# Optimization experiments

Measured on AMD Instinct MI355X. Metric: run time of the kernel, lower is better.

The kernel has to match this reference:

```python
import jax, jax.numpy as jnp
import numpy as np

D_MODEL = 1024
NUM_HEADS = 16
D_K = D_MODEL // NUM_HEADS
ROPE_THETA = 10000.0


def setup_inputs() -> dict:
    key = jax.random.key(0)
    kx, kq, kk, kv, ko = jax.random.split(key, 5)
    B, S = 2, 2048
    sigma = np.sqrt(2.0) / np.sqrt(D_MODEL + D_MODEL)
    x = jax.random.normal(kx, (B, S, D_MODEL), dtype=jnp.float32)
    Wq = jax.random.normal(kq, (D_MODEL, D_MODEL), dtype=jnp.float32) * sigma
    Wk = jax.random.normal(kk, (D_MODEL, D_MODEL), dtype=jnp.float32) * sigma
    Wv = jax.random.normal(kv, (D_MODEL, D_MODEL), dtype=jnp.float32) * sigma
    Wo = jax.random.normal(ko, (D_MODEL, D_MODEL), dtype=jnp.float32) * sigma
    return {"x": x, "Wq": Wq, "Wk": Wk, "Wv": Wv, "Wo": Wo}


def _rope(t, positions):
    # t: [B, H, S, D_K], positions: [S]
    half = jnp.arange(0, D_K, 2, dtype=jnp.float32)          # [D_K/2]
    freqs = 1.0 / (ROPE_THETA ** (half / D_K))               # [D_K/2]
    angles = positions[:, None].astype(jnp.float32) * freqs  # [S, D_K/2]
    cos = jnp.cos(angles)
    sin = jnp.sin(angles)
    t_even = t[..., 0::2]
    t_odd = t[..., 1::2]
    even_rot = t_even * cos - t_odd * sin
    odd_rot = t_even * sin + t_odd * cos
    # interleave back to [..., D_K]
    return jnp.stack([even_rot, odd_rot], axis=-1).reshape(t.shape)


def reference(x, Wq, Wk, Wv, Wo):
    B, S, _ = x.shape
    # weight layout is [d_out, d_in]: y = x @ W.T
    def proj(W):
        y = jnp.einsum('bsd,ed->bse', x, W)
        return y.reshape(B, S, NUM_HEADS, D_K).transpose(0, 2, 1, 3)  # [B,H,S,Dk]
    Q, K, V = proj(Wq), proj(Wk), proj(Wv)
    positions = jnp.arange(S)
    Q = _rope(Q, positions)
    K = _rope(K, positions)
    scale = 1.0 / jnp.sqrt(jnp.asarray(D_K, dtype=x.dtype))
    scores = jnp.einsum('bhqd,bhkd->bhqk', Q, K) * scale  # [B,H,S,S]
    causal = jnp.tril(jnp.ones((S, S), dtype=bool))
    scores = jnp.where(causal, scores, -jnp.inf)
    probs = jax.nn.softmax(scores, axis=-1)
    out = jnp.einsum('bhqk,bhkd->bhqd', probs, V)          # [B,H,S,Dk]
    out = out.transpose(0, 2, 1, 3).reshape(B, S, D_MODEL)
    return jnp.einsum('bsd,ed->bse', out, Wo)
```

## Files before the change

### kernel.cpp

```cpp
#include <hip/hip_runtime.h>
#include <hip/hip_bf16.h>
#include <math.h>

#define S_LEN   2048
#define BATCH   2
#define DMODEL  1024
#define NHEADS  16
#define DKH     64
#define MROWS   (BATCH * S_LEN)

typedef __attribute__((ext_vector_type(8))) __bf16 bf16x8;
typedef __attribute__((ext_vector_type(4))) float f32x4;
typedef __attribute__((ext_vector_type(8))) unsigned short u16x8;

__device__ __forceinline__ float bfu2f(unsigned short u) {
    union { unsigned int i; float f; } v;
    v.i = ((unsigned int)u) << 16;
    return v.f;
}

__device__ __forceinline__ unsigned short f2bfu(float f) {
    union { __bf16 h; unsigned short u; } v;
    v.h = (__bf16)f;
    return v.u;
}

#define LGKM0() __builtin_amdgcn_s_waitcnt(0xc07f)

#define SROW 40

__global__ __launch_bounds__(256) void gemm_qkv(
    const float* __restrict__ X,
    const float* __restrict__ W0, const float* __restrict__ W1, const float* __restrict__ W2,
    unsigned short* __restrict__ Yq, unsigned short* __restrict__ Yk, unsigned short* __restrict__ Yv)
{
    __shared__ __align__(16) unsigned char pool[36864];
    unsigned short* As = (unsigned short*)pool;
    unsigned short* Bs = As + 128 * SROW;

    const int tid  = threadIdx.x;
    const int wave = tid >> 6;
    const int lane = tid & 63;
    const int c    = lane & 15;
    const int quad = lane >> 4;

    const int m0 = blockIdx.y * 128;
    const int n0 = blockIdx.x * 128;
    const int w_idx = n0 >> 10;
    const int e0    = n0 & 1023;
    const float* W = (w_idx == 0) ? W0 : (w_idx == 1) ? W1 : W2;

    const int mhalf = (wave & 1) * 64;
    const int nhalf = (wave >> 1) * 64;

    f32x4 acc[4][4];
#pragma unroll
    for (int i = 0; i < 4; i++)
#pragma unroll
        for (int j = 0; j < 4; j++) acc[i][j] = (f32x4){0.f, 0.f, 0.f, 0.f};

    const int lrow = tid >> 3;
    const int lkq  = tid & 7;

    for (int k0 = 0; k0 < DMODEL; k0 += 32) {
        __syncthreads();
#pragma unroll
        for (int i = 0; i < 4; i++) {
            int row = i * 32 + lrow;
            float4 v = *(const float4*)(X + (size_t)(m0 + row) * DMODEL + k0 + lkq * 4);
            ushort4 h;
            h.x = f2bfu(v.x); h.y = f2bfu(v.y); h.z = f2bfu(v.z); h.w = f2bfu(v.w);
            *(ushort4*)(&As[row * SROW + lkq * 4]) = h;
        }
#pragma unroll
        for (int i = 0; i < 4; i++) {
            int row = i * 32 + lrow;
            float4 v = *(const float4*)(W + (size_t)(e0 + row) * DMODEL + k0 + lkq * 4);
            ushort4 h;
            h.x = f2bfu(v.x); h.y = f2bfu(v.y); h.z = f2bfu(v.z); h.w = f2bfu(v.w);
            *(ushort4*)(&Bs[row * SROW + lkq * 4]) = h;
        }
        __syncthreads();

        bf16x8 af[4], bfr[4];
#pragma unroll
        for (int mt = 0; mt < 4; mt++)
            af[mt] = *(const bf16x8*)(&As[(mhalf + mt * 16 + c) * SROW + quad * 8]);
#pragma unroll
        for (int nt = 0; nt < 4; nt++)
            bfr[nt] = *(const bf16x8*)(&Bs[(nhalf + nt * 16 + c) * SROW + quad * 8]);
#pragma unroll
        for (int mt = 0; mt < 4; mt++)
#pragma unroll
            for (int nt = 0; nt < 4; nt++)
                acc[mt][nt] = __builtin_amdgcn_mfma_f32_16x16x32_bf16(af[mt], bfr[nt], acc[mt][nt], 0, 0, 0);
    }

    __syncthreads();

    const int h = (e0 + nhalf) >> 6;
    if (w_idx < 2) {
        unsigned short* Yqk = (w_idx == 0) ? Yq : Yk;
        float* EPf = (float*)pool + wave * 16 * 68;
        const int row = lane >> 2;
        const int cg  = lane & 3;
#pragma unroll
        for (int mt = 0; mt < 4; mt++) {
            LGKM0();
#pragma unroll
            for (int nt = 0; nt < 4; nt++)
#pragma unroll
                for (int r = 0; r < 4; r++)
                    EPf[(quad * 4 + r) * 68 + nt * 16 + c] = acc[mt][nt][r];
            LGKM0();
            float fl[16];
#pragma unroll
            for (int j = 0; j < 4; j++) {
                float4 v = *(const float4*)(&EPf[row * 68 + cg * 16 + j * 4]);
                fl[j * 4 + 0] = v.x; fl[j * 4 + 1] = v.y;
                fl[j * 4 + 2] = v.z; fl[j * 4 + 3] = v.w;
            }
            int m = m0 + mhalf + mt * 16 + row;
            int s = m & (S_LEN - 1);
            int b = m >> 11;
            u16x8 o0, o1;
#pragma unroll
            for (int pi = 0; pi < 8; pi++) {
                int p = cg * 8 + pi;
                float freq  = exp2f(-(float)p * 0.41524101186092034f);
                float angle = (float)s * freq;
                float sn, cs;
                __sincosf(angle, &sn, &cs);
                float ev = fl[2 * pi], ov = fl[2 * pi + 1];
                float re = ev * cs - ov * sn;
                float ro = ev * sn + ov * cs;
                if (pi < 4) { o0[2 * pi] = f2bfu(re); o0[2 * pi + 1] = f2bfu(ro); }
                else        { o1[2 * (pi - 4)] = f2bfu(re); o1[2 * (pi - 4) + 1] = f2bfu(ro); }
            }
            unsigned short* dst = Yqk + (((size_t)(b * NHEADS + h)) * S_LEN + s) * DKH + cg * 16;
            *(u16x8*)(dst)     = o0;
            *(u16x8*)(dst + 8) = o1;
        }
    } else {
        unsigned short* EPb = (unsigned short*)pool + wave * 64 * 72;
        LGKM0();
#pragma unroll
        for (int nt = 0; nt < 4; nt++)
#pragma unroll
            for (int mt = 0; mt < 4; mt++)
#pragma unroll
                for (int r = 0; r < 4; r++)
                    EPb[(nt * 16 + c) * 72 + mt * 16 + quad * 4 + r] = f2bfu(acc[mt][nt][r]);
        LGKM0();
        int mbase = m0 + mhalf;
        int s0 = mbase & (S_LEN - 1);
        int b  = mbase >> 11;
        unsigned short* dst = Yv + (((size_t)(b * NHEADS + h)) * DKH + lane) * S_LEN + s0;
#pragma unroll
        for (int j = 0; j < 8; j++)
            *(u16x8*)(dst + j * 8) = *(const u16x8*)(&EPb[lane * 72 + j * 8]);
    }
}

__global__ __launch_bounds__(256) void gemm_wo(
    const unsigned short* __restrict__ X,
    const float* __restrict__ W,
    float* __restrict__ Yf)
{
    __shared__ __align__(16) unsigned char pool[17408];
    unsigned short* As = (unsigned short*)pool;
    unsigned short* Bs = As + 64 * SROW;

    const int tid  = threadIdx.x;
    const int wave = tid >> 6;
    const int lane = tid & 63;
    const int c    = lane & 15;
    const int quad = lane >> 4;

    const int m0 = blockIdx.y * 64;
    const int n0 = blockIdx.x * 128;

    const int mhalf = (wave & 1) * 32;
    const int nhalf = (wave >> 1) * 64;

    f32x4 acc[2][4];
#pragma unroll
    for (int i = 0; i < 2; i++)
#pragma unroll
        for (int j = 0; j < 4; j++) acc[i][j] = (f32x4){0.f, 0.f, 0.f, 0.f};

    const int lrow = tid >> 3;
    const int lkq  = tid & 7;

    ushort4 rA[2];
    float4  rB[4];
#pragma unroll
    for (int i = 0; i < 2; i++)
        rA[i] = *(const ushort4*)(X + (size_t)(m0 + i * 32 + lrow) * DMODEL + lkq * 4);
#pragma unroll
    for (int i = 0; i < 4; i++)
        rB[i] = *(const float4*)(W + (size_t)(n0 + i * 32 + lrow) * DMODEL + lkq * 4);

    for (int k0 = 0; k0 < DMODEL; k0 += 32) {
        __syncthreads();
#pragma unroll
        for (int i = 0; i < 2; i++)
            *(ushort4*)(&As[(i * 32 + lrow) * SROW + lkq * 4]) = rA[i];
#pragma unroll
        for (int i = 0; i < 4; i++) {
            ushort4 h;
            h.x = f2bfu(rB[i].x); h.y = f2bfu(rB[i].y); h.z = f2bfu(rB[i].z); h.w = f2bfu(rB[i].w);
            *(ushort4*)(&Bs[(i * 32 + lrow) * SROW + lkq * 4]) = h;
        }
        __syncthreads();

        if (k0 + 32 < DMODEL) {
#pragma unroll
            for (int i = 0; i < 2; i++)
                rA[i] = *(const ushort4*)(X + (size_t)(m0 + i * 32 + lrow) * DMODEL + k0 + 32 + lkq * 4);
#pragma unroll
            for (int i = 0; i < 4; i++)
                rB[i] = *(const float4*)(W + (size_t)(n0 + i * 32 + lrow) * DMODEL + k0 + 32 + lkq * 4);
        }

        bf16x8 af[2], bfr[4];
#pragma unroll
        for (int mt = 0; mt < 2; mt++)
            af[mt] = *(const bf16x8*)(&As[(mhalf + mt * 16 + c) * SROW + quad * 8]);
#pragma unroll
        for (int nt = 0; nt < 4; nt++)
            bfr[nt] = *(const bf16x8*)(&Bs[(nhalf + nt * 16 + c) * SROW + quad * 8]);
#pragma unroll
        for (int mt = 0; mt < 2; mt++)
#pragma unroll
            for (int nt = 0; nt < 4; nt++)
                acc[mt][nt] = __builtin_amdgcn_mfma_f32_16x16x32_bf16(af[mt], bfr[nt], acc[mt][nt], 0, 0, 0);
    }

    __syncthreads();

    float* EPf = (float*)pool + wave * 16 * 68;
    const int row = lane >> 2;
    const int cg  = lane & 3;
#pragma unroll
    for (int mt = 0; mt < 2; mt++) {
        LGKM0();
#pragma unroll
        for (int nt = 0; nt < 4; nt++)
#pragma unroll
            for (int r = 0; r < 4; r++)
                EPf[(quad * 4 + r) * 68 + nt * 16 + c] = acc[mt][nt][r];
        LGKM0();
        int m = m0 + mhalf + mt * 16 + row;
        float* dst = Yf + (size_t)m * DMODEL + n0 + nhalf + cg * 16;
#pragma unroll
        for (int j = 0; j < 4; j++)
            *(float4*)(dst + j * 4) = *(const float4*)(&EPf[row * 68 + cg * 16 + j * 4]);
    }
}

__global__ __launch_bounds__(256, 4) void attn_mfma(
    const unsigned short* __restrict__ Q,
    const unsigned short* __restrict__ K,
    const unsigned short* __restrict__ Vt,
    unsigned short* __restrict__ A)
{
    __shared__ unsigned short Ks[64 * 72];
    __shared__ unsigned short Vs[64 * 72];
    __shared__ unsigned short Plds[4][16 * 72];

    const int tid  = threadIdx.x;
    const int wave = tid >> 6;
    const int lane = tid & 63;
    const int c    = lane & 15;
    const int quad = lane >> 4;

    const int bh = blockIdx.x;
    const int b  = bh >> 4;
    const int h  = bh & 15;
    const int qb = (int)(gridDim.y - 1) - (int)blockIdx.y;
    const int q0 = qb * 64 + wave * 16;

    const unsigned short* Qb = Q  + (size_t)bh * S_LEN * DKH;
    const unsigned short* Kb = K  + (size_t)bh * S_LEN * DKH;
    const unsigned short* Vb = Vt + (size_t)bh * DKH * S_LEN;

    bf16x8 qf0 = *(const bf16x8*)(Qb + (q0 + c) * DKH + quad * 8);
    bf16x8 qf1 = *(const bf16x8*)(Qb + (q0 + c) * DKH + 32 + quad * 8);

    f32x4 o[4];
#pragma unroll
    for (int dt = 0; dt < 4; dt++) o[dt] = (f32x4){0.f,0.f,0.f,0.f};
    float l[4] = {0.f, 0.f, 0.f, 0.f};

    unsigned short* Pw = &Plds[wave][0];

    const int nkb     = qb + 1;
    const int kb_full = (q0 >= 63) ? (((q0 - 63) >> 6) + 1) : 0;

    const int srow = tid >> 2;
    const int scol = (tid & 3) * 16;

    uint4 gK0 = *(const uint4*)(Kb + (size_t)srow * DKH + scol);
    uint4 gK1 = *(const uint4*)(Kb + (size_t)srow * DKH + scol + 8);
    uint4 gV0 = *(const uint4*)(Vb + (size_t)srow * S_LEN + scol);
    uint4 gV1 = *(const uint4*)(Vb + (size_t)srow * S_LEN + scol + 8);

    for (int kb = 0; kb < nkb; kb++) {
        const int k0 = kb * 64;
        __syncthreads();
        *(uint4*)(&Ks[srow * 72 + scol])     = gK0;
        *(uint4*)(&Ks[srow * 72 + scol + 8]) = gK1;
        *(uint4*)(&Vs[srow * 72 + scol])     = gV0;
        *(uint4*)(&Vs[srow * 72 + scol + 8]) = gV1;
        __syncthreads();
        if (kb + 1 < nkb) {
            gK0 = *(const uint4*)(Kb + (size_t)(k0 + 64 + srow) * DKH + scol);
            gK1 = *(const uint4*)(Kb + (size_t)(k0 + 64 + srow) * DKH + scol + 8);
            gV0 = *(const uint4*)(Vb + (size_t)srow * S_LEN + k0 + 64 + scol);
            gV1 = *(const uint4*)(Vb + (size_t)srow * S_LEN + k0 + 64 + scol + 8);
        }

        f32x4 s[4];
#pragma unroll
        for (int t = 0; t < 4; t++) {
            bf16x8 kA = *(const bf16x8*)(&Ks[(t * 16 + c) * 72 + quad * 8]);
            bf16x8 kB = *(const bf16x8*)(&Ks[(t * 16 + c) * 72 + 32 + quad * 8]);
            f32x4 z = {0.f,0.f,0.f,0.f};
            z = __builtin_amdgcn_mfma_f32_16x16x32_bf16(qf0, kA, z, 0, 0, 0);
            z = __builtin_amdgcn_mfma_f32_16x16x32_bf16(qf1, kB, z, 0, 0, 0);
            s[t] = z;
        }

        if (kb < kb_full) {
#pragma unroll
            for (int t = 0; t < 4; t++)
#pragma unroll
                for (int r = 0; r < 4; r++) {
                    unsigned short pb = f2bfu(__expf(s[t][r] * 0.125f));
                    Pw[(quad * 4 + r) * 72 + t * 16 + c] = pb;
                    l[r] += bfu2f(pb);
                }
        } else {
#pragma unroll
            for (int t = 0; t < 4; t++)
#pragma unroll
                for (int r = 0; r < 4; r++) {
                    int qrow = q0 + quad * 4 + r;
                    float e = (k0 + t * 16 + c <= qrow) ? __expf(s[t][r] * 0.125f) : 0.0f;
                    unsigned short pb = f2bfu(e);
                    Pw[(quad * 4 + r) * 72 + t * 16 + c] = pb;
                    l[r] += bfu2f(pb);
                }
        }
        LGKM0();

        bf16x8 pf0 = *(const bf16x8*)(Pw + c * 72 + quad * 8);
        bf16x8 pf1 = *(const bf16x8*)(Pw + c * 72 + 32 + quad * 8);

#pragma unroll
        for (int dt = 0; dt < 4; dt++) {
            bf16x8 vA = *(const bf16x8*)(&Vs[(dt * 16 + c) * 72 + quad * 8]);
            bf16x8 vB = *(const bf16x8*)(&Vs[(dt * 16 + c) * 72 + 32 + quad * 8]);
            o[dt] = __builtin_amdgcn_mfma_f32_16x16x32_bf16(pf0, vA, o[dt], 0, 0, 0);
            o[dt] = __builtin_amdgcn_mfma_f32_16x16x32_bf16(pf1, vB, o[dt], 0, 0, 0);
        }
    }

#pragma unroll
    for (int m = 1; m < 16; m <<= 1) {
#pragma unroll
        for (int r = 0; r < 4; r++) l[r] += __shfl_xor(l[r], m, 64);
    }

#pragma unroll
    for (int r = 0; r < 4; r++) {
        float inv = 1.0f / l[r];
        int s = q0 + quad * 4 + r;
        unsigned short* Ap = A + ((size_t)b * S_LEN + s) * DMODEL + h * DKH;
        Ap[0 * 16 + c] = f2bfu(o[0][r] * inv);
        Ap[1 * 16 + c] = f2bfu(o[1][r] * inv);
        Ap[2 * 16 + c] = f2bfu(o[2][r] * inv);
        Ap[3 * 16 + c] = f2bfu(o[3][r] * inv);
    }
}

extern "C" void kernel_launch(void* const* d_in, const int* in_sizes, int n_in,
                              void* d_out, int out_size, void* d_ws, size_t ws_size,
                              hipStream_t stream) {
    const float* x  = (const float*)d_in[0];
    const float* Wq = (const float*)d_in[1];
    const float* Wk = (const float*)d_in[2];
    const float* Wv = (const float*)d_in[3];
    const float* Wo = (const float*)d_in[4];
    float* out = (float*)d_out;

    unsigned short* Qw = (unsigned short*)d_ws;
    unsigned short* Kw = Qw + (size_t)MROWS * DMODEL;
    unsigned short* Vw = Kw + (size_t)MROWS * DMODEL;
    unsigned short* Aw = Vw + (size_t)MROWS * DMODEL;

    gemm_qkv<<<dim3(3 * DMODEL / 128, MROWS / 128), 256, 0, stream>>>(
        x, Wq, Wk, Wv, Qw, Kw, Vw);

    attn_mfma<<<dim3(NHEADS * BATCH, S_LEN / 64), 256, 0, stream>>>(Qw, Kw, Vw, Aw);

    gemm_wo<<<dim3(DMODEL / 128, MROWS / 64), 256, 0, stream>>>(Aw, Wo, out);
}
```

Measured before the change: 196.5 us.

## Pre-convert QKV weights to bf16 and widen GEMM K-tile to 64

A new kernel converts Wq/Wk/Wv to bf16 once per call into workspace, so the QKV GEMM loads half-size bf16 weight tiles instead of converting fp32 in every block. Both GEMMs move to a 64-wide K step with a padded LDS row stride of 72, halving the number of barrier-separated iterations. The Wo GEMM drops its register prefetch of the next tile, which may expose global-load latency. The converted weights share workspace with the attention output buffer, which is safe only because they are consumed before attention writes it.

```diff
diff --git a/kernel.cpp b/kernel.cpp
--- a/kernel.cpp
+++ b/kernel.cpp
@@ -27,16 +27,28 @@
 
 #define LGKM0() __builtin_amdgcn_s_waitcnt(0xc07f)
 
-#define SROW 40
+__global__ __launch_bounds__(256) void cvt_w(
+    const float* __restrict__ W0, const float* __restrict__ W1, const float* __restrict__ W2,
+    unsigned short* __restrict__ Wb)
+{
+    const float* W = (blockIdx.y == 0) ? W0 : (blockIdx.y == 1) ? W1 : W2;
+    size_t idx = ((size_t)blockIdx.x * 256 + threadIdx.x) * 8;
+    float4 a = *(const float4*)(W + idx);
+    float4 b = *(const float4*)(W + idx + 4);
+    u16x8 h;
+    h[0] = f2bfu(a.x); h[1] = f2bfu(a.y); h[2] = f2bfu(a.z); h[3] = f2bfu(a.w);
+    h[4] = f2bfu(b.x); h[5] = f2bfu(b.y); h[6] = f2bfu(b.z); h[7] = f2bfu(b.w);
+    *(u16x8*)(Wb + (size_t)blockIdx.y * (DMODEL * DMODEL) + idx) = h;
+}
 
 __global__ __launch_bounds__(256) void gemm_qkv(
     const float* __restrict__ X,
-    const float* __restrict__ W0, const float* __restrict__ W1, const float* __restrict__ W2,
+    const unsigned short* __restrict__ Wb,
     unsigned short* __restrict__ Yq, unsigned short* __restrict__ Yk, unsigned short* __restrict__ Yv)
 {
     __shared__ __align__(16) unsigned char pool[36864];
     unsigned short* As = (unsigned short*)pool;
-    unsigned short* Bs = As + 128 * SROW;
+    unsigned short* Bs = As + 128 * 72;
 
     const int tid  = threadIdx.x;
     const int wave = tid >> 6;
@@ -48,7 +60,7 @@
     const int n0 = blockIdx.x * 128;
     const int w_idx = n0 >> 10;
     const int e0    = n0 & 1023;
-    const float* W = (w_idx == 0) ? W0 : (w_idx == 1) ? W1 : W2;
+    const unsigned short* Wsrc = Wb + (size_t)w_idx * (DMODEL * DMODEL);
 
     const int mhalf = (wave & 1) * 64;
     const int nhalf = (wave >> 1) * 64;
@@ -59,41 +71,41 @@
 #pragma unroll
         for (int j = 0; j < 4; j++) acc[i][j] = (f32x4){0.f, 0.f, 0.f, 0.f};
 
-    const int lrow = tid >> 3;
-    const int lkq  = tid & 7;
-
-    for (int k0 = 0; k0 < DMODEL; k0 += 32) {
+    const int srow = tid >> 3;
+    const int scol = (tid & 7) * 8;
+
+    for (int k0 = 0; k0 < DMODEL; k0 += 64) {
         __syncthreads();
 #pragma unroll
         for (int i = 0; i < 4; i++) {
-            int row = i * 32 + lrow;
-            float4 v = *(const float4*)(X + (size_t)(m0 + row) * DMODEL + k0 + lkq * 4);
-            ushort4 h;
-            h.x = f2bfu(v.x); h.y = f2bfu(v.y); h.z = f2bfu(v.z); h.w = f2bfu(v.w);
-            *(ushort4*)(&As[row * SROW + lkq * 4]) = h;
-        }
-#pragma unroll
-        for (int i = 0; i < 4; i++) {
-            int row = i * 32 + lrow;
-            float4 v = *(const float4*)(W + (size_t)(e0 + row) * DMODEL + k0 + lkq * 4);
-            ushort4 h;
-            h.x = f2bfu(v.x); h.y = f2bfu(v.y); h.z = f2bfu(v.z); h.w = f2bfu(v.w);
-            *(ushort4*)(&Bs[row * SROW + lkq * 4]) = h;
-        }
-        __syncthreads();
-
-        bf16x8 af[4], bfr[4];
-#pragma unroll
-        for (int mt = 0; mt < 4; mt++)
-            af[mt] = *(const bf16x8*)(&As[(mhalf + mt * 16 + c) * SROW + quad * 8]);
-#pragma unroll
-        for (int nt = 0; nt < 4; nt++)
-            bfr[nt] = *(const bf16x8*)(&Bs[(nhalf + nt * 16 + c) * SROW + quad * 8]);
-#pragma unroll
-        for (int mt = 0; mt < 4; mt++)
+            int row = i * 32 + srow;
+            const float* p = X + (size_t)(m0 + row) * DMODEL + k0 + scol;
+            float4 va = *(const float4*)(p);
+            float4 vb = *(const float4*)(p + 4);
+            u16x8 h;
+            h[0] = f2bfu(va.x); h[1] = f2bfu(va.y); h[2] = f2bfu(va.z); h[3] = f2bfu(va.w);
+            h[4] = f2bfu(vb.x); h[5] = f2bfu(vb.y); h[6] = f2bfu(vb.z); h[7] = f2bfu(vb.w);
+            *(u16x8*)(&As[row * 72 + scol]) = h;
+            *(u16x8*)(&Bs[row * 72 + scol]) =
+                *(const u16x8*)(Wsrc + (size_t)(e0 + row) * DMODEL + k0 + scol);
+        }
+        __syncthreads();
+
+#pragma unroll
+        for (int half = 0; half < 2; half++) {
+            bf16x8 af[4], bfr[4];
+#pragma unroll
+            for (int mt = 0; mt < 4; mt++)
+                af[mt] = *(const bf16x8*)(&As[(mhalf + mt * 16 + c) * 72 + half * 32 + quad * 8]);
 #pragma unroll
             for (int nt = 0; nt < 4; nt++)
-                acc[mt][nt] = __builtin_amdgcn_mfma_f32_16x16x32_bf16(af[mt], bfr[nt], acc[mt][nt], 0, 0, 0);
+                bfr[nt] = *(const bf16x8*)(&Bs[(nhalf + nt * 16 + c) * 72 + half * 32 + quad * 8]);
+#pragma unroll
+            for (int mt = 0; mt < 4; mt++)
+#pragma unroll
+                for (int nt = 0; nt < 4; nt++)
+                    acc[mt][nt] = __builtin_amdgcn_mfma_f32_16x16x32_bf16(af[mt], bfr[nt], acc[mt][nt], 0, 0, 0);
+        }
     }
 
     __syncthreads();
@@ -167,9 +179,9 @@
     const float* __restrict__ W,
     float* __restrict__ Yf)
 {
-    __shared__ __align__(16) unsigned char pool[17408];
+    __shared__ __align__(16) unsigned char pool[27648];
     unsigned short* As = (unsigned short*)pool;
-    unsigned short* Bs = As + 64 * SROW;
+    unsigned short* Bs = As + 64 * 72;
 
     const int tid  = threadIdx.x;
     const int wave = tid >> 6;
@@ -189,52 +201,45 @@
 #pragma unroll
         for (int j = 0; j < 4; j++) acc[i][j] = (f32x4){0.f, 0.f, 0.f, 0.f};
 
-    const int lrow = tid >> 3;
-    const int lkq  = tid & 7;
-
-    ushort4 rA[2];
-    float4  rB[4];
-#pragma unroll
-    for (int i = 0; i < 2; i++)
-        rA[i] = *(const ushort4*)(X + (size_t)(m0 + i * 32 + lrow) * DMODEL + lkq * 4);
-#pragma unroll
-    for (int i = 0; i < 4; i++)
-        rB[i] = *(const float4*)(W + (size_t)(n0 + i * 32 + lrow) * DMODEL + lkq * 4);
-
-    for (int k0 = 0; k0 < DMODEL; k0 += 32) {
-        __syncthreads();
-#pragma unroll
-        for (int i = 0; i < 2; i++)
-            *(ushort4*)(&As[(i * 32 + lrow) * SROW + lkq * 4]) = rA[i];
+    const int srow = tid >> 3;
+    const int scol = (tid & 7) * 8;
+
+    for (int k0 = 0; k0 < DMODEL; k0 += 64) {
+        __syncthreads();
+#pragma unroll
+        for (int i = 0; i < 2; i++) {
+            int row = i * 32 + srow;
+            *(u16x8*)(&As[row * 72 + scol]) =
+                *(const u16x8*)(X + (size_t)(m0 + row) * DMODEL + k0 + scol);
+        }
 #pragma unroll
         for (int i = 0; i < 4; i++) {
-            ushort4 h;
-            h.x = f2bfu(rB[i].x); h.y = f2bfu(rB[i].y); h.z = f2bfu(rB[i].z); h.w = f2bfu(rB[i].w);
-            *(ushort4*)(&Bs[(i * 32 + lrow) * SROW + lkq * 4]) = h;
-        }
-        __syncthreads();
-
-        if (k0 + 32 < DMODEL) {
-#pragma unroll
-            for (int i = 0; i < 2; i++)
-                rA[i] = *(const ushort4*)(X + (size_t)(m0 + i * 32 + lrow) * DMODEL + k0 + 32 + lkq * 4);
-#pragma unroll
-            for (int i = 0; i < 4; i++)
-                rB[i] = *(const float4*)(W + (size_t)(n0 + i * 32 + lrow) * DMODEL + k0 + 32 + lkq * 4);
-        }
-
-        bf16x8 af[2], bfr[4];
-#pragma unroll
-        for (int mt = 0; mt < 2; mt++)
-            af[mt] = *(const bf16x8*)(&As[(mhalf + mt * 16 + c) * SROW + quad * 8]);
-#pragma unroll
-        for (int nt = 0; nt < 4; nt++)
-            bfr[nt] = *(const bf16x8*)(&Bs[(nhalf + nt * 16 + c) * SROW + quad * 8]);
-#pragma unroll
-        for (int mt = 0; mt < 2; mt++)
+            int row = i * 32 + srow;
+            const float* p = W + (size_t)(n0 + row) * DMODEL + k0 + scol;
+            float4 va = *(const float4*)(p);
+            float4 vb = *(const float4*)(p + 4);
+            u16x8 h;
+            h[0] = f2bfu(va.x); h[1] = f2bfu(va.y); h[2] = f2bfu(va.z); h[3] = f2bfu(va.w);
+            h[4] = f2bfu(vb.x); h[5] = f2bfu(vb.y); h[6] = f2bfu(vb.z); h[7] = f2bfu(vb.w);
+            *(u16x8*)(&Bs[row * 72 + scol]) = h;
+        }
+        __syncthreads();
+
+#pragma unroll
+        for (int half = 0; half < 2; half++) {
+            bf16x8 af[2], bfr[4];
+#pragma unroll
+            for (int mt = 0; mt < 2; mt++)
+                af[mt] = *(const bf16x8*)(&As[(mhalf + mt * 16 + c) * 72 + half * 32 + quad * 8]);
 #pragma unroll
             for (int nt = 0; nt < 4; nt++)
-                acc[mt][nt] = __builtin_amdgcn_mfma_f32_16x16x32_bf16(af[mt], bfr[nt], acc[mt][nt], 0, 0, 0);
+                bfr[nt] = *(const bf16x8*)(&Bs[(nhalf + nt * 16 + c) * 72 + half * 32 + quad * 8]);
+#pragma unroll
+            for (int mt = 0; mt < 2; mt++)
+#pragma unroll
+                for (int nt = 0; nt < 4; nt++)
+                    acc[mt][nt] = __builtin_amdgcn_mfma_f32_16x16x32_bf16(af[mt], bfr[nt], acc[mt][nt], 0, 0, 0);
+        }
     }
 
     __syncthreads();
@@ -398,10 +403,13 @@
     unsigned short* Qw = (unsigned short*)d_ws;
     unsigned short* Kw = Qw + (size_t)MROWS * DMODEL;
     unsigned short* Vw = Kw + (size_t)MROWS * DMODEL;
-    unsigned short* Aw = Vw + (size_t)MROWS * DMODEL;
+    unsigned short* Wb = Vw + (size_t)MROWS * DMODEL;
+    unsigned short* Aw = Wb;
+
+    cvt_w<<<dim3(DMODEL * DMODEL / (256 * 8), 3), 256, 0, stream>>>(Wq, Wk, Wv, Wb);
 
     gemm_qkv<<<dim3(3 * DMODEL / 128, MROWS / 128), 256, 0, stream>>>(
-        x, Wq, Wk, Wv, Qw, Kw, Vw);
+        x, Wb, Qw, Kw, Vw);
 
     attn_mfma<<<dim3(NHEADS * BATCH, S_LEN / 64), 256, 0, stream>>>(Qw, Kw, Vw, Aw);
 
```

After: 200.9 us. +2.2%, slower.
